# Performance work log

Hardware: AMD Instinct MI355X
Metric: run time of the kernel (lower is better)

## Reference

```python
import jax, jax.numpy as jnp
import numpy as np

B, L, D, H, FF = 8, 512, 1024, 16, 1024
HD = D // H
EPS = 1e-5
ROPE_BASE = 10000.0
ROPE_DIM = D  # module passes dim=embed_dim (not head_dim) to RotaryPositionalEmbeddings


def _layer_norm(x, g, b):
    m = jnp.mean(x, axis=-1, keepdims=True)
    v = jnp.var(x, axis=-1, keepdims=True)
    return (x - m) * jax.lax.rsqrt(v + EPS) * g + b


def _rope(x):
    # x: [B, H, L, HD]; interleaved-pair rotation, frequencies base**(-2i/ROPE_DIM)
    half = HD // 2
    inv_freq = 1.0 / (ROPE_BASE ** (jnp.arange(half, dtype=jnp.float32) * 2.0 / ROPE_DIM))
    ang = jnp.arange(L, dtype=jnp.float32)[:, None] * inv_freq[None, :]  # [L, half]
    cos = jnp.cos(ang)
    sin = jnp.sin(ang)
    xr = x.reshape(*x.shape[:-1], half, 2)
    x1, x2 = xr[..., 0], xr[..., 1]
    out = jnp.stack([x1 * cos - x2 * sin, x1 * sin + x2 * cos], axis=-1)
    return out.reshape(x.shape).astype(x.dtype)


def setup_inputs() -> dict:
    key = jax.random.key(0)
    ks = jax.random.split(key, 16)
    sd = 0.02
    n = lambda k, shape: (jax.random.normal(k, shape, dtype=jnp.float32) * sd)
    return {
        "input_ids": jax.random.normal(ks[0], (B, L, D), dtype=jnp.float32),
        "Wq": n(ks[1], (FF, D)), "bq": jnp.zeros((D,), jnp.float32),
        "Wk": n(ks[2], (FF, D)), "bk": jnp.zeros((D,), jnp.float32),
        "Wv": n(ks[3], (FF, D)), "bv": jnp.zeros((D,), jnp.float32),
        "Wo": n(ks[4], (D, D)),  "bo": jnp.zeros((D,), jnp.float32),
        "Wf": n(ks[5], (D, FF)), "bf": jnp.zeros((FF,), jnp.float32),
        "g_ffn": jnp.ones((D,), jnp.float32), "b_ffn": jnp.zeros((D,), jnp.float32),
        "g_attn": jnp.ones((FF,), jnp.float32), "b_attn": jnp.zeros((FF,), jnp.float32),
    }


def reference(input_ids, Wq, bq, Wk, bk, Wv, bv, Wo, bo, Wf, bf,
              g_ffn, b_ffn, g_attn, b_attn):
    # FFN branch: computed then DISCARDED in the original source (x is overwritten).
    _ffn_dead = jax.nn.relu(_layer_norm(input_ids, g_ffn, b_ffn) @ Wf + bf)  # noqa: F841

    x = _layer_norm(input_ids, g_attn, b_attn)  # pre_attn_norm applied to input_ids
    q = (x @ Wq + bq).reshape(B, L, H, HD).transpose(0, 2, 1, 3)  # [B,H,L,HD]
    k = (x @ Wk + bk).reshape(B, L, H, HD).transpose(0, 2, 1, 3)
    v = (x @ Wv + bv).reshape(B, L, H, HD).transpose(0, 2, 1, 3)
    q = _rope(q)
    k = _rope(k)

    scale = 1.0 / np.sqrt(HD).astype(np.float32)
    scores = jnp.einsum("bhqd,bhkd->bhqk", q, k) * scale  # [B,H,L,L]
    attn = jax.nn.softmax(scores, axis=-1)
    o = jnp.einsum("bhqk,bhkd->bhqd", attn, v)
    o = o.transpose(0, 2, 1, 3).reshape(B, L, D)
    return input_ids + (o @ Wo + bo)
```

## Files before the change

kernel.cpp:

```cpp
#include <hip/hip_runtime.h>

typedef unsigned short ushort_t;
typedef short bf16x8 __attribute__((ext_vector_type(8)));
typedef float f32x4 __attribute__((ext_vector_type(4)));

#define B_ 8
#define L_ 512
#define D_ 1024
#define H_ 16
#define M_ 4096

__device__ __forceinline__ ushort_t f2bf(float f) {
  union { float f; unsigned u; } v; v.f = f;
  unsigned r = v.u + 0x7FFFu + ((v.u >> 16) & 1u);
  return (ushort_t)(r >> 16);
}

__device__ __forceinline__ void gl_lds16(const ushort_t* g, ushort_t* s) {
  __builtin_amdgcn_global_load_lds((const __attribute__((address_space(1))) void*)(g),
                                   (__attribute__((address_space(3))) void*)(s), 16, 0, 0);
}

__global__ __launch_bounds__(256) void prep_kernel(const float* __restrict__ x,
                                                   const float* __restrict__ g,
                                                   const float* __restrict__ b,
                                                   ushort_t* __restrict__ xn,
                                                   float2* __restrict__ csb,
                                                   const float* __restrict__ w0,
                                                   const float* __restrict__ w1,
                                                   const float* __restrict__ w2,
                                                   const float* __restrict__ w3,
                                                   ushort_t* __restrict__ wt) {
  __shared__ float tile[32][33];
  int blk = blockIdx.x, t = threadIdx.x;
  if (blk < 1024) {
    int row = blk * 4 + (t >> 6);
    int lane = t & 63;
    const float4* xr = (const float4*)(x + (size_t)row * D_);
    float4 v[4];
    float s = 0.f, s2 = 0.f;
#pragma unroll
    for (int j = 0; j < 4; ++j) {
      v[j] = xr[j * 64 + lane];
      s  += v[j].x + v[j].y + v[j].z + v[j].w;
      s2 += v[j].x * v[j].x + v[j].y * v[j].y + v[j].z * v[j].z + v[j].w * v[j].w;
    }
#pragma unroll
    for (int m = 1; m < 64; m <<= 1) { s += __shfl_xor(s, m); s2 += __shfl_xor(s2, m); }
    float mean = s * (1.0f / D_);
    float var  = s2 * (1.0f / D_) - mean * mean;
    float rs   = rsqrtf(var + 1e-5f);
    unsigned long long* outp = (unsigned long long*)(xn + (size_t)row * D_);
#pragma unroll
    for (int j = 0; j < 4; ++j) {
      float4 gg = ((const float4*)g)[j * 64 + lane];
      float4 bb = ((const float4*)b)[j * 64 + lane];
      unsigned long long pk =
          (unsigned long long)f2bf((v[j].x - mean) * rs * gg.x + bb.x)
        | ((unsigned long long)f2bf((v[j].y - mean) * rs * gg.y + bb.y) << 16)
        | ((unsigned long long)f2bf((v[j].z - mean) * rs * gg.z + bb.z) << 32)
        | ((unsigned long long)f2bf((v[j].w - mean) * rs * gg.w + bb.w) << 48);
      outp[j * 64 + lane] = pk;
    }
  } else if (blk < 1088) {
    int idx = (blk - 1024) * 256 + t;
    int l = idx >> 5, i = idx & 31;
    float inv = powf(10000.0f, (-2.0f * (float)i) / 1024.0f);
    float ang = (float)l * inv;
    csb[idx] = make_float2(cosf(ang), sinf(ang));
  } else {
    int wb = blk - 1088;
    int z = wb >> 10;
    const float* W = (z == 0) ? w0 : (z == 1) ? w1 : (z == 2) ? w2 : w3;
    ushort_t* WT = wt + ((size_t)z << 20);
    int rem = wb & 1023;
    int by = rem >> 5, bx = rem & 31;
    int tx = t & 31, ty = t >> 5;
    int k0 = by * 32, n0 = bx * 32;
#pragma unroll
    for (int j = 0; j < 4; ++j)
      tile[ty + 8 * j][tx] = W[(size_t)(k0 + ty + 8 * j) * 1024 + n0 + tx];
    __syncthreads();
#pragma unroll
    for (int j = 0; j < 4; ++j)
      WT[(size_t)(n0 + ty + 8 * j) * 1024 + k0 + tx] = f2bf(tile[tx][ty + 8 * j]);
  }
}

__global__ __launch_bounds__(256) void gemm_qkv_kernel(const ushort_t* __restrict__ xn,
                                                       const ushort_t* __restrict__ wt,
                                                       const float* __restrict__ bq,
                                                       const float* __restrict__ bk,
                                                       const float* __restrict__ bv,
                                                       ushort_t* __restrict__ qb,
                                                       ushort_t* __restrict__ kb,
                                                       ushort_t* __restrict__ vt,
                                                       const float2* __restrict__ csb) {
  __shared__ ushort_t As[64 * 64];
  __shared__ ushort_t Bs[128 * 64];
  int t = threadIdx.x, l = t & 63, w = t >> 6, lr = l & 15, lg = l >> 4;
  int hid = blockIdx.x;
  int xcd = hid & 7, lid = hid >> 3;
  int by = (xcd >> 1) * 16 + lid / 12;
  int bx = (xcd & 1) * 12 + lid % 12;
  int m0 = by * 64;
  int n0g = bx * 128;
  int z = n0g >> 10;
  int n0 = n0g & 1023;
  const float* bias = (z == 0) ? bq : (z == 1) ? bk : bv;
  int wr = w >> 1, wc = w & 1;
  const int sr8 = l >> 3;
  const int scol = ((l & 7) ^ sr8) * 8;

  f32x4 acc[2][4] = {};

  for (int k0 = 0; k0 < 1024; k0 += 64) {
    gl_lds16(&xn[(size_t)(m0 + w * 16 + sr8) * 1024 + k0 + scol], &As[(w * 16) * 64]);
    gl_lds16(&xn[(size_t)(m0 + w * 16 + 8 + sr8) * 1024 + k0 + scol], &As[(w * 16 + 8) * 64]);
    gl_lds16(&wt[(size_t)(n0g + w * 32 + sr8) * 1024 + k0 + scol], &Bs[(w * 32) * 64]);
    gl_lds16(&wt[(size_t)(n0g + w * 32 + 8 + sr8) * 1024 + k0 + scol], &Bs[(w * 32 + 8) * 64]);
    gl_lds16(&wt[(size_t)(n0g + w * 32 + 16 + sr8) * 1024 + k0 + scol], &Bs[(w * 32 + 16) * 64]);
    gl_lds16(&wt[(size_t)(n0g + w * 32 + 24 + sr8) * 1024 + k0 + scol], &Bs[(w * 32 + 24) * 64]);
    __syncthreads();
#pragma unroll
    for (int kk = 0; kk < 2; ++kk) {
      bf16x8 a[2], bfr[4];
#pragma unroll
      for (int mi = 0; mi < 2; ++mi)
        a[mi] = *(const bf16x8*)&As[(wr * 32 + mi * 16 + lr) * 64 + (((kk * 4 + lg) ^ (lr & 7)) << 3)];
#pragma unroll
      for (int ni = 0; ni < 4; ++ni)
        bfr[ni] = *(const bf16x8*)&Bs[(wc * 64 + ni * 16 + lr) * 64 + (((kk * 4 + lg) ^ (lr & 7)) << 3)];
#pragma unroll
      for (int mi = 0; mi < 2; ++mi)
#pragma unroll
        for (int ni = 0; ni < 4; ++ni)
          acc[mi][ni] = __builtin_amdgcn_mfma_f32_16x16x32_bf16(a[mi], bfr[ni], acc[mi][ni], 0, 0, 0);
    }
    __syncthreads();
  }

  if (z < 2) {
    ushort_t* outp = (z == 0) ? qb : kb;
    const float sc = (z == 0) ? 0.125f : 1.0f;
#pragma unroll
    for (int mi = 0; mi < 2; ++mi) {
      int rowb = m0 + wr * 32 + mi * 16 + lg * 4;
#pragma unroll
      for (int ni = 0; ni < 4; ++ni) {
        int col = n0 + wc * 64 + ni * 16 + lr;
        float bvv = bias[col];
        int ii = (col & 63) >> 1;
        int codd = col & 1;
#pragma unroll
        for (int r = 0; r < 4; ++r) {
          float val = acc[mi][ni][r] + bvv;
          float par = __shfl_xor(val, 1);
          float2 cs = csb[((rowb + r) & 511) * 32 + ii];
          float y = codd ? (par * cs.y + val * cs.x) : (val * cs.x - par * cs.y);
          outp[(size_t)(rowb + r) * 1024 + col] = f2bf(y * sc);
        }
      }
    }
  } else {
#pragma unroll
    for (int mi = 0; mi < 2; ++mi) {
      int rowb = m0 + wr * 32 + mi * 16 + lg * 4;
      int bidx = rowb >> 9, l0 = rowb & 511;
#pragma unroll
      for (int ni = 0; ni < 4; ++ni) {
        int col = n0 + wc * 64 + ni * 16 + lr;
        float bvv = bias[col];
        unsigned long long pk =
            (unsigned long long)f2bf(acc[mi][ni][0] + bvv)
          | ((unsigned long long)f2bf(acc[mi][ni][1] + bvv) << 16)
          | ((unsigned long long)f2bf(acc[mi][ni][2] + bvv) << 32)
          | ((unsigned long long)f2bf(acc[mi][ni][3] + bvv) << 48);
        *(unsigned long long*)&vt[((size_t)(bidx << 10) + col) * 512 + l0] = pk;
      }
    }
  }
}

__global__ __launch_bounds__(64) void gemm_o_kernel(const ushort_t* __restrict__ A,
                                                    const ushort_t* __restrict__ Bt,
                                                    const float* __restrict__ bias,
                                                    const float* __restrict__ res,
                                                    float* __restrict__ out) {
  __shared__ ushort_t As[32 * 64];
  __shared__ ushort_t Bs[64 * 64];
  int l = threadIdx.x, lr = l & 15, lg = l >> 4;
  int hid = blockIdx.x;
  int xcd = hid & 7, lid = hid >> 3;
  int by = xcd * 16 + (lid >> 4);
  int bx = lid & 15;
  int m0 = by * 32, n0 = bx * 64;
  const int sr8 = l >> 3;
  const int scol = ((l & 7) ^ sr8) * 8;

  f32x4 acc[2][4] = {};

  for (int k0 = 0; k0 < 1024; k0 += 64) {
#pragma unroll
    for (int i = 0; i < 4; ++i)
      gl_lds16(&A[(size_t)(m0 + i * 8 + sr8) * 1024 + k0 + scol], &As[(i * 8) * 64]);
#pragma unroll
    for (int i = 0; i < 8; ++i)
      gl_lds16(&Bt[(size_t)(n0 + i * 8 + sr8) * 1024 + k0 + scol], &Bs[(i * 8) * 64]);
    __syncthreads();
#pragma unroll
    for (int kk = 0; kk < 2; ++kk) {
      bf16x8 a[2], bfr[4];
#pragma unroll
      for (int mi = 0; mi < 2; ++mi)
        a[mi] = *(const bf16x8*)&As[(mi * 16 + lr) * 64 + (((kk * 4 + lg) ^ (lr & 7)) << 3)];
#pragma unroll
      for (int ni = 0; ni < 4; ++ni)
        bfr[ni] = *(const bf16x8*)&Bs[(ni * 16 + lr) * 64 + (((kk * 4 + lg) ^ (lr & 7)) << 3)];
#pragma unroll
      for (int mi = 0; mi < 2; ++mi)
#pragma unroll
        for (int ni = 0; ni < 4; ++ni)
          acc[mi][ni] = __builtin_amdgcn_mfma_f32_16x16x32_bf16(a[mi], bfr[ni], acc[mi][ni], 0, 0, 0);
    }
    __syncthreads();
  }

#pragma unroll
  for (int mi = 0; mi < 2; ++mi) {
    int rowb = m0 + mi * 16 + lg * 4;
#pragma unroll
    for (int ni = 0; ni < 4; ++ni) {
      int col = n0 + ni * 16 + lr;
      float bvv = bias[col];
#pragma unroll
      for (int r = 0; r < 4; ++r) {
        size_t off = (size_t)(rowb + r) * 1024 + col;
        out[off] = acc[mi][ni][r] + bvv + res[off];
      }
    }
  }
}

__global__ __launch_bounds__(256) void attn_kernel(const ushort_t* __restrict__ q,
                                                   const ushort_t* __restrict__ k,
                                                   const ushort_t* __restrict__ vt,
                                                   ushort_t* __restrict__ o) {
  __shared__ ushort_t Ks[2][64 * 64];
  __shared__ ushort_t Vs[2][64 * 64];
  __shared__ ushort_t Ps[4][16 * 64];
  int t = threadIdx.x, l = t & 63, w = t >> 6, lr = l & 15, lg = l >> 4;
  int blk = blockIdx.x;
  int bh = blk & 127, qt = blk >> 7;
  int b = bh >> 4, h = bh & 15;
  const int srow = l >> 3;
  const int scol = ((l & 7) ^ (srow & 7)) * 8;

  bf16x8 qf[2];
  {
    size_t qrow = (size_t)(b * 512 + qt * 64 + w * 16 + lr);
#pragma unroll
    for (int kh = 0; kh < 2; ++kh)
      qf[kh] = *(const bf16x8*)&q[qrow * 1024 + h * 64 + kh * 32 + lg * 8];
  }

  f32x4 oacc[4] = {};
  float mrun = -1e30f;
  float lrun = 0.f;

#define STAGE(buf, kv0)                                                              \
  {                                                                                  \
    _Pragma("unroll")                                                                \
    for (int j = 0; j < 2; ++j) {                                                    \
      gl_lds16(&k[(size_t)(b * 512 + (kv0) + w * 16 + j * 8 + srow) * 1024 + h * 64 + scol], \
               &Ks[buf][(w * 16 + j * 8) * 64]);                                     \
      gl_lds16(&vt[((size_t)bh * 64 + w * 16 + j * 8 + srow) * 512 + (kv0) + scol],  \
               &Vs[buf][(w * 16 + j * 8) * 64]);                                     \
    }                                                                                \
  }

  STAGE(0, 0);
  __syncthreads();
  int cur = 0;
  for (int it = 0; it < 8; ++it) {
    if (it < 7) { STAGE(cur ^ 1, (it + 1) * 64); }
    f32x4 st[4] = {};
#pragma unroll
    for (int kh = 0; kh < 2; ++kh)
#pragma unroll
      for (int kn = 0; kn < 4; ++kn) {
        bf16x8 kf = *(const bf16x8*)&Ks[cur][(kn * 16 + lr) * 64 + (((kh * 4 + lg) ^ (lr & 7)) << 3)];
        st[kn] = __builtin_amdgcn_mfma_f32_16x16x32_bf16(kf, qf[kh], st[kn], 0, 0, 0);
      }
    float mx = st[0][0];
#pragma unroll
    for (int kn = 0; kn < 4; ++kn)
#pragma unroll
      for (int r = 0; r < 4; ++r) mx = fmaxf(mx, st[kn][r]);
    mx = fmaxf(mx, __shfl_xor(mx, 16));
    mx = fmaxf(mx, __shfl_xor(mx, 32));
    float mn = mrun, al = 1.0f;
    if (!__all(mx <= mrun + 8.0f)) {
      mn = fmaxf(mrun, mx);
      al = __expf(mrun - mn);
      mrun = mn;
#pragma unroll
      for (int f = 0; f < 4; ++f) {
        oacc[f][0] *= al; oacc[f][1] *= al;
        oacc[f][2] *= al; oacc[f][3] *= al;
      }
    }
    float sm = 0.f;
#pragma unroll
    for (int kn = 0; kn < 4; ++kn) {
      float p0 = __expf(st[kn][0] - mn);
      float p1 = __expf(st[kn][1] - mn);
      float p2 = __expf(st[kn][2] - mn);
      float p3 = __expf(st[kn][3] - mn);
      sm += p0 + p1 + p2 + p3;
      int kvb = kn * 16 + 4 * lg;
      unsigned long long pk =
          (unsigned long long)f2bf(p0)
        | ((unsigned long long)f2bf(p1) << 16)
        | ((unsigned long long)f2bf(p2) << 32)
        | ((unsigned long long)f2bf(p3) << 48);
      *(unsigned long long*)&Ps[w][lr * 64 + (((kvb >> 3) ^ (lr & 7)) << 3) + (kvb & 7)] = pk;
    }
    sm += __shfl_xor(sm, 16);
    sm += __shfl_xor(sm, 32);
    lrun = lrun * al + sm;

    asm volatile("s_waitcnt lgkmcnt(0)" ::: "memory");
    __builtin_amdgcn_sched_barrier(0);
#pragma unroll
    for (int kk = 0; kk < 2; ++kk) {
      int sl = (((kk * 4 + lg) ^ (lr & 7)) << 3);
      bf16x8 pb = *(const bf16x8*)&Ps[w][lr * 64 + sl];
#pragma unroll
      for (int f = 0; f < 4; ++f) {
        bf16x8 vf = *(const bf16x8*)&Vs[cur][(f * 16 + lr) * 64 + sl];
        oacc[f] = __builtin_amdgcn_mfma_f32_16x16x32_bf16(vf, pb, oacc[f], 0, 0, 0);
      }
    }
    __syncthreads();
    cur ^= 1;
  }
  {
    float inv = 1.0f / lrun;
    size_t qrow = (size_t)(b * 512 + qt * 64 + w * 16 + lr);
#pragma unroll
    for (int f = 0; f < 4; ++f) {
      unsigned long long pk =
          (unsigned long long)f2bf(oacc[f][0] * inv)
        | ((unsigned long long)f2bf(oacc[f][1] * inv) << 16)
        | ((unsigned long long)f2bf(oacc[f][2] * inv) << 32)
        | ((unsigned long long)f2bf(oacc[f][3] * inv) << 48);
      *(unsigned long long*)&o[qrow * 1024 + h * 64 + f * 16 + 4 * lg] = pk;
    }
  }
#undef STAGE
}

extern "C" void kernel_launch(void* const* d_in, const int* in_sizes, int n_in,
                              void* d_out, int out_size, void* d_ws, size_t ws_size,
                              hipStream_t stream) {
  const float* input_ids = (const float*)d_in[0];
  const float* Wq = (const float*)d_in[1];
  const float* bq = (const float*)d_in[2];
  const float* Wk = (const float*)d_in[3];
  const float* bk = (const float*)d_in[4];
  const float* Wv = (const float*)d_in[5];
  const float* bv = (const float*)d_in[6];
  const float* Wo = (const float*)d_in[7];
  const float* bo = (const float*)d_in[8];
  const float* g_attn = (const float*)d_in[13];
  const float* b_attn = (const float*)d_in[14];
  float* out = (float*)d_out;

  char* ws = (char*)d_ws;
  const size_t MB = 1024 * 1024;
  ushort_t* wt = (ushort_t*)(ws);
  ushort_t* xn = (ushort_t*)(ws + 8 * MB);
  ushort_t* qb = (ushort_t*)(ws + 16 * MB);
  ushort_t* kb = (ushort_t*)(ws + 24 * MB);
  ushort_t* vt = (ushort_t*)(ws + 32 * MB);
  float2* csb  = (float2*)(ws + 40 * MB);

  prep_kernel<<<5184, 256, 0, stream>>>(input_ids, g_attn, b_attn, xn, csb,
                                        Wq, Wk, Wv, Wo, wt);
  gemm_qkv_kernel<<<1536, 256, 0, stream>>>(xn, wt, bq, bk, bv, qb, kb, vt, csb);
  attn_kernel<<<1024, 256, 0, stream>>>(qb, kb, vt, xn);
  gemm_o_kernel<<<2048, 64, 0, stream>>>(xn, wt + 3 * MB, bo, input_ids, out);
}
```

Before: 90.86 us.

## Enlarge QKV GEMM tile to 128x128 and use 32x32x16 MFMA

The QKV projection GEMM now computes a 128x128 output tile per block instead of 64x128. Each wave now issues 32x32x16 bf16 MFMAs on 64x64 sub-tiles, where it previously used 16x16x32 ones. The epilogues for RoPE and the V transpose are rewritten for the 32x32 accumulator layout, and the grid is halved to 768 blocks. This raises operand reuse per LDS load and cuts LDS read traffic, at the cost of fewer blocks for the CUs, more LDS per block and more accumulator registers.

Result: slower. 97.58 us (+7.4%).

```diff
diff --git a/kernel.cpp b/kernel.cpp
--- a/kernel.cpp
+++ b/kernel.cpp
@@ -3,6 +3,7 @@
 typedef unsigned short ushort_t;
 typedef short bf16x8 __attribute__((ext_vector_type(8)));
 typedef float f32x4 __attribute__((ext_vector_type(4)));
+typedef float f32x16 __attribute__((ext_vector_type(16)));
 
 #define B_ 8
 #define L_ 512
@@ -96,14 +97,15 @@
                                                        ushort_t* __restrict__ kb,
                                                        ushort_t* __restrict__ vt,
                                                        const float2* __restrict__ csb) {
-  __shared__ ushort_t As[64 * 64];
+  __shared__ ushort_t As[128 * 64];
   __shared__ ushort_t Bs[128 * 64];
-  int t = threadIdx.x, l = t & 63, w = t >> 6, lr = l & 15, lg = l >> 4;
+  int t = threadIdx.x, l = t & 63, w = t >> 6;
+  int lc = l & 31, lh = l >> 5;
   int hid = blockIdx.x;
   int xcd = hid & 7, lid = hid >> 3;
-  int by = (xcd >> 1) * 16 + lid / 12;
+  int by = (xcd >> 1) * 8 + lid / 12;
   int bx = (xcd & 1) * 12 + lid % 12;
-  int m0 = by * 64;
+  int m0 = by * 128;
   int n0g = bx * 128;
   int z = n0g >> 10;
   int n0 = n0g & 1023;
@@ -112,30 +114,35 @@
   const int sr8 = l >> 3;
   const int scol = ((l & 7) ^ sr8) * 8;
 
-  f32x4 acc[2][4] = {};
+  f32x16 acc[2][2] = {};
 
   for (int k0 = 0; k0 < 1024; k0 += 64) {
-    gl_lds16(&xn[(size_t)(m0 + w * 16 + sr8) * 1024 + k0 + scol], &As[(w * 16) * 64]);
-    gl_lds16(&xn[(size_t)(m0 + w * 16 + 8 + sr8) * 1024 + k0 + scol], &As[(w * 16 + 8) * 64]);
-    gl_lds16(&wt[(size_t)(n0g + w * 32 + sr8) * 1024 + k0 + scol], &Bs[(w * 32) * 64]);
-    gl_lds16(&wt[(size_t)(n0g + w * 32 + 8 + sr8) * 1024 + k0 + scol], &Bs[(w * 32 + 8) * 64]);
-    gl_lds16(&wt[(size_t)(n0g + w * 32 + 16 + sr8) * 1024 + k0 + scol], &Bs[(w * 32 + 16) * 64]);
-    gl_lds16(&wt[(size_t)(n0g + w * 32 + 24 + sr8) * 1024 + k0 + scol], &Bs[(w * 32 + 24) * 64]);
-    __syncthreads();
-#pragma unroll
-    for (int kk = 0; kk < 2; ++kk) {
-      bf16x8 a[2], bfr[4];
+#pragma unroll
+    for (int i = 0; i < 4; ++i) {
+      gl_lds16(&xn[(size_t)(m0 + w * 32 + i * 8 + sr8) * 1024 + k0 + scol],
+               &As[(w * 32 + i * 8) * 64]);
+      gl_lds16(&wt[(size_t)(n0g + w * 32 + i * 8 + sr8) * 1024 + k0 + scol],
+               &Bs[(w * 32 + i * 8) * 64]);
+    }
+    __syncthreads();
+#pragma unroll
+    for (int ks = 0; ks < 4; ++ks) {
+      bf16x8 a[2], bb[2];
+#pragma unroll
+      for (int mi = 0; mi < 2; ++mi) {
+        int row = wr * 64 + mi * 32 + lc;
+        a[mi] = *(const bf16x8*)&As[row * 64 + (((ks * 2 + lh) ^ (row & 7)) << 3)];
+      }
+#pragma unroll
+      for (int ni = 0; ni < 2; ++ni) {
+        int row = wc * 64 + ni * 32 + lc;
+        bb[ni] = *(const bf16x8*)&Bs[row * 64 + (((ks * 2 + lh) ^ (row & 7)) << 3)];
+      }
 #pragma unroll
       for (int mi = 0; mi < 2; ++mi)
-        a[mi] = *(const bf16x8*)&As[(wr * 32 + mi * 16 + lr) * 64 + (((kk * 4 + lg) ^ (lr & 7)) << 3)];
-#pragma unroll
-      for (int ni = 0; ni < 4; ++ni)
-        bfr[ni] = *(const bf16x8*)&Bs[(wc * 64 + ni * 16 + lr) * 64 + (((kk * 4 + lg) ^ (lr & 7)) << 3)];
-#pragma unroll
-      for (int mi = 0; mi < 2; ++mi)
-#pragma unroll
-        for (int ni = 0; ni < 4; ++ni)
-          acc[mi][ni] = __builtin_amdgcn_mfma_f32_16x16x32_bf16(a[mi], bfr[ni], acc[mi][ni], 0, 0, 0);
+#pragma unroll
+        for (int ni = 0; ni < 2; ++ni)
+          acc[mi][ni] = __builtin_amdgcn_mfma_f32_32x32x16_bf16(a[mi], bb[ni], acc[mi][ni], 0, 0, 0);
     }
     __syncthreads();
   }
@@ -145,38 +152,44 @@
     const float sc = (z == 0) ? 0.125f : 1.0f;
 #pragma unroll
     for (int mi = 0; mi < 2; ++mi) {
-      int rowb = m0 + wr * 32 + mi * 16 + lg * 4;
-#pragma unroll
-      for (int ni = 0; ni < 4; ++ni) {
-        int col = n0 + wc * 64 + ni * 16 + lr;
+#pragma unroll
+      for (int ni = 0; ni < 2; ++ni) {
+        int col = n0 + wc * 64 + ni * 32 + lc;
         float bvv = bias[col];
         int ii = (col & 63) >> 1;
         int codd = col & 1;
 #pragma unroll
-        for (int r = 0; r < 4; ++r) {
-          float val = acc[mi][ni][r] + bvv;
-          float par = __shfl_xor(val, 1);
-          float2 cs = csb[((rowb + r) & 511) * 32 + ii];
-          float y = codd ? (par * cs.y + val * cs.x) : (val * cs.x - par * cs.y);
-          outp[(size_t)(rowb + r) * 1024 + col] = f2bf(y * sc);
+        for (int j = 0; j < 4; ++j) {
+#pragma unroll
+          for (int rr = 0; rr < 4; ++rr) {
+            int row = m0 + wr * 64 + mi * 32 + lh * 4 + 8 * j + rr;
+            float val = acc[mi][ni][4 * j + rr] + bvv;
+            float par = __shfl_xor(val, 1);
+            float2 cs = csb[(row & 511) * 32 + ii];
+            float y = codd ? (par * cs.y + val * cs.x) : (val * cs.x - par * cs.y);
+            outp[(size_t)row * 1024 + col] = f2bf(y * sc);
+          }
         }
       }
     }
   } else {
 #pragma unroll
     for (int mi = 0; mi < 2; ++mi) {
-      int rowb = m0 + wr * 32 + mi * 16 + lg * 4;
-      int bidx = rowb >> 9, l0 = rowb & 511;
-#pragma unroll
-      for (int ni = 0; ni < 4; ++ni) {
-        int col = n0 + wc * 64 + ni * 16 + lr;
+#pragma unroll
+      for (int ni = 0; ni < 2; ++ni) {
+        int col = n0 + wc * 64 + ni * 32 + lc;
         float bvv = bias[col];
-        unsigned long long pk =
-            (unsigned long long)f2bf(acc[mi][ni][0] + bvv)
-          | ((unsigned long long)f2bf(acc[mi][ni][1] + bvv) << 16)
-          | ((unsigned long long)f2bf(acc[mi][ni][2] + bvv) << 32)
-          | ((unsigned long long)f2bf(acc[mi][ni][3] + bvv) << 48);
-        *(unsigned long long*)&vt[((size_t)(bidx << 10) + col) * 512 + l0] = pk;
+#pragma unroll
+        for (int j = 0; j < 4; ++j) {
+          int rowb = m0 + wr * 64 + mi * 32 + lh * 4 + 8 * j;
+          int bidx = rowb >> 9, l0 = rowb & 511;
+          unsigned long long pk =
+              (unsigned long long)f2bf(acc[mi][ni][4 * j + 0] + bvv)
+            | ((unsigned long long)f2bf(acc[mi][ni][4 * j + 1] + bvv) << 16)
+            | ((unsigned long long)f2bf(acc[mi][ni][4 * j + 2] + bvv) << 32)
+            | ((unsigned long long)f2bf(acc[mi][ni][4 * j + 3] + bvv) << 48);
+          *(unsigned long long*)&vt[((size_t)(bidx << 10) + col) * 512 + l0] = pk;
+        }
       }
     }
   }
@@ -388,7 +401,7 @@
 
   prep_kernel<<<5184, 256, 0, stream>>>(input_ids, g_attn, b_attn, xn, csb,
                                         Wq, Wk, Wv, Wo, wt);
-  gemm_qkv_kernel<<<1536, 256, 0, stream>>>(xn, wt, bq, bk, bv, qb, kb, vt, csb);
+  gemm_qkv_kernel<<<768, 256, 0, stream>>>(xn, wt, bq, bk, bv, qb, kb, vt, csb);
   attn_kernel<<<1024, 256, 0, stream>>>(qb, kb, vt, xn);
   gemm_o_kernel<<<2048, 64, 0, stream>>>(xn, wt + 3 * MB, bo, input_ids, out);
 }
```
